# Performance work log

Hardware: AMD Instinct MI355X
Metric: run time of the kernel (lower is better)

The kernel has to match this reference:

```python
import jax, jax.numpy as jnp
import numpy as np

D_MODEL = 1024
D_HIDDEN = 4096
NUM_EXPERTS = 8
K_ACTIVE = 2


def setup_inputs() -> dict:
    key = jax.random.key(0)
    ks = jax.random.split(key, 8)
    x = jax.random.normal(ks[0], (1, 2048, D_MODEL), dtype=jnp.float32)
    gate_w = jax.random.normal(ks[1], (D_MODEL, NUM_EXPERTS), dtype=jnp.float32) * 0.02
    gate_b = jnp.zeros((NUM_EXPERTS,), dtype=jnp.float32)
    w1 = jax.random.normal(ks[2], (NUM_EXPERTS, D_MODEL, D_HIDDEN), dtype=jnp.float32) * 0.02
    b1 = jnp.zeros((NUM_EXPERTS, D_HIDDEN), dtype=jnp.float32)
    w2 = jax.random.normal(ks[3], (NUM_EXPERTS, D_HIDDEN, D_MODEL), dtype=jnp.float32) * 0.02
    b2 = jnp.zeros((NUM_EXPERTS, D_MODEL), dtype=jnp.float32)
    return {"x": x, "gate_w": gate_w, "gate_b": gate_b,
            "w1": w1, "b1": b1, "w2": w2, "b2": b2}


def reference(x, gate_w, gate_b, w1, b1, w2, b2):
    B, S, D = x.shape
    xf = x.reshape(-1, D)                                    # [T, D]
    logits = xf @ gate_w + gate_b                            # [T, E]
    top_w, top_idx = jax.lax.top_k(logits, K_ACTIVE)         # [T, K]
    top_w = jax.nn.softmax(top_w, axis=-1)                   # softmax over selected experts
    # combine-weight per expert: sum over k slots of one-hot(idx) * weight -> [T, E]
    gates = jnp.sum(jax.nn.one_hot(top_idx, NUM_EXPERTS, dtype=xf.dtype) * top_w[..., None], axis=1)
    # expert FFN applied per expert (dropout is identity in eval): gelu is exact (erf), matching torch nn.GELU default
    h = jax.nn.gelu(jnp.einsum('td,edh->teh', xf, w1) + b1[None], approximate=False)  # [T, E, H]
    y = jnp.einsum('teh,ehd->ted', h, w2) + b2[None]         # [T, E, D]
    out = jnp.einsum('ted,te->td', y, gates)                 # weighted combine of selected experts
    return out.reshape(B, S, D)
```

## Files before the change

### kernel.cpp

```cpp
#include <hip/hip_runtime.h>
#include <stdint.h>

typedef unsigned short u16;
typedef __attribute__((ext_vector_type(8))) short s16x8;
typedef __attribute__((ext_vector_type(8))) u16  u16x8;
typedef __attribute__((ext_vector_type(4))) float f32x4;

#define T_TOKENS 2048
#define DM 1024
#define DH 4096
#define NE 8
#define BM 128
#define BN 128
#define BK 64
#define MAXSLOTS (T_TOKENS*2 + NE*BM)
#define ROWBLK (MAXSLOTS/BM)

__device__ __forceinline__ u16 f2bf(float f) {
    union { float ff; uint32_t u; } v; v.ff = f;
    uint32_t r = v.u + 0x7fffu + ((v.u >> 16) & 1u);
    return (u16)(r >> 16);
}

#define GLOAD_LDS16(gsrc, ldst) \
    __builtin_amdgcn_global_load_lds((const __attribute__((address_space(1))) uint32_t*)(gsrc), \
                                     (__attribute__((address_space(3))) uint32_t*)(ldst), 16, 0, 0)

__global__ void k_convert(const float* __restrict__ x, u16* __restrict__ xbf,
                          int* __restrict__ ctrl) {
    int i = blockIdx.x * blockDim.x + threadIdx.x;
    const f32x4* xv = (const f32x4*)x;
    f32x4 a = xv[2*i], b = xv[2*i+1];
    u16x8 o;
    o[0]=f2bf(a[0]); o[1]=f2bf(a[1]); o[2]=f2bf(a[2]); o[3]=f2bf(a[3]);
    o[4]=f2bf(b[0]); o[5]=f2bf(b[1]); o[6]=f2bf(b[2]); o[7]=f2bf(b[3]);
    ((u16x8*)xbf)[i] = o;
    if (blockIdx.x == 0 && threadIdx.x < 32) ctrl[threadIdx.x] = 0;
}

__global__ void __launch_bounds__(64) k_gate(const float* __restrict__ x,
                                             const float* __restrict__ gw,
                                             const float* __restrict__ gb,
                                             int* __restrict__ cnt,
                                             int* __restrict__ tt_idx,
                                             float* __restrict__ tt_w) {
    const int t = blockIdx.x;
    const int lane = threadIdx.x;
    float acc[NE] = {0.f,0.f,0.f,0.f,0.f,0.f,0.f,0.f};
    const float* xr = x + (size_t)t * DM;
    #pragma unroll
    for (int c = 0; c < DM/64; ++c) {
        float xv = xr[lane + 64*c];
        const float* g = gw + (size_t)(lane + 64*c) * NE;
        #pragma unroll
        for (int e = 0; e < NE; ++e) acc[e] += xv * g[e];
    }
    #pragma unroll
    for (int e = 0; e < NE; ++e) {
        #pragma unroll
        for (int off = 32; off >= 1; off >>= 1)
            acc[e] += __shfl_xor(acc[e], off, 64);
    }
    if (lane == 0) {
        float l[NE];
        #pragma unroll
        for (int e = 0; e < NE; ++e) l[e] = acc[e] + gb[e];
        int i0 = 0;
        #pragma unroll
        for (int e = 1; e < NE; ++e) if (l[e] > l[i0]) i0 = e;
        int i1 = (i0 == 0) ? 1 : 0;
        #pragma unroll
        for (int e = 0; e < NE; ++e) if (e != i0 && l[e] > l[i1]) i1 = e;
        float m  = l[i0];
        float w0 = expf(l[i0] - m), w1 = expf(l[i1] - m);
        float s = w0 + w1; w0 /= s; w1 /= s;
        tt_idx[t*2] = i0; tt_idx[t*2+1] = i1;
        tt_w[t*2] = w0;  tt_w[t*2+1] = w1;
        atomicAdd(&cnt[i0], 1); atomicAdd(&cnt[i1], 1);
    }
}

__global__ void k_offsets(const int* __restrict__ cnt, int* __restrict__ fill,
                          int* __restrict__ off) {
    if (threadIdx.x == 0 && blockIdx.x == 0) {
        int a = 0;
        for (int e = 0; e < NE; ++e) {
            off[e] = a;
            a += (cnt[e] + BM - 1) / BM * BM;
            fill[e] = 0;
        }
        off[NE] = a;
    }
}

__global__ void k_scatter(const int* __restrict__ tt_idx, const float* __restrict__ tt_w,
                          const int* __restrict__ off, int* __restrict__ fill,
                          int* __restrict__ slot_token, float* __restrict__ slot_gate) {
    int t = blockIdx.x * blockDim.x + threadIdx.x;
    if (t >= T_TOKENS) return;
    #pragma unroll
    for (int k = 0; k < 2; ++k) {
        int e = tt_idx[t*2+k];
        int pos = off[e] + atomicAdd(&fill[e], 1);
        slot_token[pos] = t;
        slot_gate[pos]  = tt_w[t*2+k];
    }
}

__global__ void __launch_bounds__(256) k_ffn1(
    const u16* __restrict__ xbf, const float* __restrict__ w1,
    const float* __restrict__ b1, const int* __restrict__ slot_token,
    const int* __restrict__ off, u16* __restrict__ h)
{
    __shared__ u16 As[BM*BK];
    __shared__ u16 Bs[BN*BK];
    const int rb = blockIdx.y, cb = blockIdx.x;
    const int total = off[NE];
    const int r0 = rb * BM;
    if (r0 >= total) return;
    int e = 0;
    while (e < NE-1 && off[e+1] <= r0) e++;
    const float* Bsrc = w1 + (size_t)e * DM * DH;
    const float* be   = b1 + (size_t)e * DH;

    const int tid = threadIdx.x;
    const int lane = tid & 63, wid = tid >> 6;
    const int wr = wid >> 1, wc = wid & 1;

    const u16* gA[4];
    #pragma unroll
    for (int i = 0; i < 4; ++i) {
        int row = wid*32 + i*8 + (lane >> 3);
        int g = (lane & 7) ^ (row & 7);
        int tok = slot_token[r0 + row];
        gA[i] = xbf + (size_t)tok * DM + g*8;
    }
    const int tc = tid & 31, tr = tid >> 5;
    const float* gB = Bsrc + (size_t)(tr*8) * DH + cb*BN + tc*4;

    f32x4 acc[4][4];
    #pragma unroll
    for (int m = 0; m < 4; ++m)
        #pragma unroll
        for (int n = 0; n < 4; ++n) acc[m][n] = (f32x4){0.f,0.f,0.f,0.f};

    for (int kt = 0; kt < DM/BK; ++kt) {
        #pragma unroll
        for (int i = 0; i < 4; ++i)
            GLOAD_LDS16(gA[i] + kt*BK, &As[(wid*32 + i*8)*BK]);
        f32x4 bv[8];
        #pragma unroll
        for (int j = 0; j < 8; ++j)
            bv[j] = *(const f32x4*)(gB + (size_t)(kt*BK + j) * DH);
        #pragma unroll
        for (int c = 0; c < 4; ++c) {
            int n = tc*4 + c;
            int sl = tr ^ (n & 7);
            s16x8 pk;
            #pragma unroll
            for (int j = 0; j < 8; ++j) pk[j] = (short)f2bf(bv[j][c]);
            *(s16x8*)&Bs[n*BK + sl*8] = pk;
        }
        __syncthreads();
        #pragma unroll
        for (int ko = 0; ko < 2; ++ko) {
            s16x8 af[4], bfr[4];
            #pragma unroll
            for (int m = 0; m < 4; ++m) {
                int row = wr*64 + m*16 + (lane & 15);
                int sl = (ko*4 + (lane >> 4)) ^ (row & 7);
                af[m] = *(const s16x8*)&As[row*BK + sl*8];
            }
            #pragma unroll
            for (int n = 0; n < 4; ++n) {
                int col = wc*64 + n*16 + (lane & 15);
                int sl = (ko*4 + (lane >> 4)) ^ (col & 7);
                bfr[n] = *(const s16x8*)&Bs[col*BK + sl*8];
            }
            #pragma unroll
            for (int m = 0; m < 4; ++m)
                #pragma unroll
                for (int n = 0; n < 4; ++n)
                    acc[m][n] = __builtin_amdgcn_mfma_f32_16x16x32_bf16(af[m], bfr[n], acc[m][n], 0, 0, 0);
        }
        __syncthreads();
    }
    #pragma unroll
    for (int n = 0; n < 4; ++n) {
        int col = cb*BN + wc*64 + n*16 + (lane & 15);
        float bb = be[col];
        #pragma unroll
        for (int m = 0; m < 4; ++m) {
            int rbase = r0 + wr*64 + m*16 + (lane >> 4)*4;
            #pragma unroll
            for (int i = 0; i < 4; ++i) {
                float v = acc[m][n][i] + bb;
                float gv = 0.5f * v * (1.0f + erff(v * 0.70710678118654752f));
                h[(size_t)(rbase + i)*DH + col] = f2bf(gv);
            }
        }
    }
}

__global__ void __launch_bounds__(256) k_ffn2(
    const u16* __restrict__ h, const float* __restrict__ w2,
    const float* __restrict__ b2, const int* __restrict__ slot_token,
    const float* __restrict__ slot_gate, const int* __restrict__ off,
    float* __restrict__ out)
{
    __shared__ u16 As[BM*BK];
    __shared__ u16 Bs[BN*BK];
    const int rb = blockIdx.y, cb = blockIdx.x;
    const int total = off[NE];
    const int r0 = rb * BM;
    if (r0 >= total) return;
    int e = 0;
    while (e < NE-1 && off[e+1] <= r0) e++;
    const float* Bsrc = w2 + (size_t)e * DH * DM;
    const float* be   = b2 + (size_t)e * DM;

    const int tid = threadIdx.x;
    const int lane = tid & 63, wid = tid >> 6;
    const int wr = wid >> 1, wc = wid & 1;

    const u16* gA[4];
    #pragma unroll
    for (int i = 0; i < 4; ++i) {
        int row = wid*32 + i*8 + (lane >> 3);
        int g = (lane & 7) ^ (row & 7);
        gA[i] = h + (size_t)(r0 + row) * DH + g*8;
    }
    const int tc = tid & 31, tr = tid >> 5;
    const float* gB = Bsrc + (size_t)(tr*8) * DM + cb*BN + tc*4;

    f32x4 acc[4][4];
    #pragma unroll
    for (int m = 0; m < 4; ++m)
        #pragma unroll
        for (int n = 0; n < 4; ++n) acc[m][n] = (f32x4){0.f,0.f,0.f,0.f};

    for (int kt = 0; kt < DH/BK; ++kt) {
        #pragma unroll
        for (int i = 0; i < 4; ++i)
            GLOAD_LDS16(gA[i] + kt*BK, &As[(wid*32 + i*8)*BK]);
        f32x4 bv[8];
        #pragma unroll
        for (int j = 0; j < 8; ++j)
            bv[j] = *(const f32x4*)(gB + (size_t)(kt*BK + j) * DM);
        #pragma unroll
        for (int c = 0; c < 4; ++c) {
            int n = tc*4 + c;
            int sl = tr ^ (n & 7);
            s16x8 pk;
            #pragma unroll
            for (int j = 0; j < 8; ++j) pk[j] = (short)f2bf(bv[j][c]);
            *(s16x8*)&Bs[n*BK + sl*8] = pk;
        }
        __syncthreads();
        #pragma unroll
        for (int ko = 0; ko < 2; ++ko) {
            s16x8 af[4], bfr[4];
            #pragma unroll
            for (int m = 0; m < 4; ++m) {
                int row = wr*64 + m*16 + (lane & 15);
                int sl = (ko*4 + (lane >> 4)) ^ (row & 7);
                af[m] = *(const s16x8*)&As[row*BK + sl*8];
            }
            #pragma unroll
            for (int n = 0; n < 4; ++n) {
                int col = wc*64 + n*16 + (lane & 15);
                int sl = (ko*4 + (lane >> 4)) ^ (col & 7);
                bfr[n] = *(const s16x8*)&Bs[col*BK + sl*8];
            }
            #pragma unroll
            for (int m = 0; m < 4; ++m)
                #pragma unroll
                for (int n = 0; n < 4; ++n)
                    acc[m][n] = __builtin_amdgcn_mfma_f32_16x16x32_bf16(af[m], bfr[n], acc[m][n], 0, 0, 0);
        }
        __syncthreads();
    }
    float bb[4];
    #pragma unroll
    for (int n = 0; n < 4; ++n) bb[n] = be[cb*BN + wc*64 + n*16 + (lane & 15)];
    #pragma unroll
    for (int m = 0; m < 4; ++m) {
        #pragma unroll
        for (int i = 0; i < 4; ++i) {
            int s = r0 + wr*64 + m*16 + (lane >> 4)*4 + i;
            int tok = slot_token[s];
            float g = slot_gate[s];
            if (g != 0.0f) {
                float* orow = out + (size_t)tok * DM + cb*BN + wc*64;
                #pragma unroll
                for (int n = 0; n < 4; ++n)
                    atomicAdd(orow + n*16 + (lane & 15), g * (acc[m][n][i] + bb[n]));
            }
        }
    }
}

extern "C" void kernel_launch(void* const* d_in, const int* in_sizes, int n_in,
                              void* d_out, int out_size, void* d_ws, size_t ws_size,
                              hipStream_t stream)
{
    (void)in_sizes; (void)n_in; (void)out_size; (void)ws_size;
    const float* x  = (const float*)d_in[0];
    const float* gw = (const float*)d_in[1];
    const float* gb = (const float*)d_in[2];
    const float* w1 = (const float*)d_in[3];
    const float* b1 = (const float*)d_in[4];
    const float* w2 = (const float*)d_in[5];
    const float* b2 = (const float*)d_in[6];
    float* out = (float*)d_out;
    char* ws = (char*)d_ws;

    u16*   xbf        = (u16*)(ws);
    u16*   h          = (u16*)(ws + 4194304);
    int*   slot_token = (int*)(ws + 46137344);
    float* slot_gate  = (float*)(ws + 46157824);
    int*   tt_idx     = (int*)(ws + 46178304);
    float* tt_w       = (float*)(ws + 46194688);
    int*   ctrl       = (int*)(ws + 46211072);
    int* cnt = ctrl; int* fill = ctrl + 8; int* offs = ctrl + 16;

    hipMemsetAsync(slot_token, 0, 2 * MAXSLOTS * 4, stream);
    hipMemsetAsync(out, 0, (size_t)T_TOKENS * DM * sizeof(float), stream);

    k_convert<<<(T_TOKENS*DM/8 + 255)/256, 256, 0, stream>>>(x, xbf, ctrl);
    k_gate<<<T_TOKENS, 64, 0, stream>>>(x, gw, gb, cnt, tt_idx, tt_w);
    k_offsets<<<1, 64, 0, stream>>>(cnt, fill, offs);
    k_scatter<<<(T_TOKENS + 255)/256, 256, 0, stream>>>(tt_idx, tt_w, offs, fill, slot_token, slot_gate);
    k_ffn1<<<dim3(DH/BN, ROWBLK), 256, 0, stream>>>(xbf, w1, b1, slot_token, offs, h);
    k_ffn2<<<dim3(DM/BN, ROWBLK), 256, 0, stream>>>(h, w2, b2, slot_token, slot_gate, offs, out);
}
```

Before: 351.1 us.

## Pre-transpose expert weights to bf16 and stream them via LDS-direct loads

```diff
diff --git a/kernel.cpp b/kernel.cpp
--- a/kernel.cpp
+++ b/kernel.cpp
@@ -4,6 +4,7 @@
 typedef unsigned short u16;
 typedef __attribute__((ext_vector_type(8))) short s16x8;
 typedef __attribute__((ext_vector_type(8))) u16  u16x8;
+typedef __attribute__((ext_vector_type(4))) u16  u16x4;
 typedef __attribute__((ext_vector_type(4))) float f32x4;
 
 #define T_TOKENS 2048
@@ -12,6 +13,7 @@
 #define NE 8
 #define BM 128
 #define BN 128
+#define BN2 64
 #define BK 64
 #define MAXSLOTS (T_TOKENS*2 + NE*BM)
 #define ROWBLK (MAXSLOTS/BM)
@@ -38,6 +40,33 @@
     if (blockIdx.x == 0 && threadIdx.x < 32) ctrl[threadIdx.x] = 0;
 }
 
+__global__ void __launch_bounds__(256) k_transpose(const float* __restrict__ src,
+                                                   u16* __restrict__ dst,
+                                                   int K, int N) {
+    __shared__ float tile[64][65];
+    const int e = blockIdx.z;
+    const int n0 = blockIdx.x * 64, k0 = blockIdx.y * 64;
+    const float* s = src + (size_t)e * K * N;
+    u16* d = dst + (size_t)e * K * N;
+    const int tx = threadIdx.x & 15, ty = threadIdx.x >> 4;
+    #pragma unroll
+    for (int j = 0; j < 4; ++j) {
+        int r = ty * 4 + j;
+        f32x4 v = *(const f32x4*)(s + (size_t)(k0 + r) * N + n0 + tx * 4);
+        tile[r][tx*4+0] = v[0]; tile[r][tx*4+1] = v[1];
+        tile[r][tx*4+2] = v[2]; tile[r][tx*4+3] = v[3];
+    }
+    __syncthreads();
+    #pragma unroll
+    for (int j = 0; j < 4; ++j) {
+        int n = ty * 4 + j;
+        u16x4 w;
+        #pragma unroll
+        for (int c = 0; c < 4; ++c) w[c] = f2bf(tile[tx*4+c][n]);
+        *(u16x4*)(d + (size_t)(n0 + n) * K + k0 + tx * 4) = w;
+    }
+}
+
 __global__ void __launch_bounds__(64) k_gate(const float* __restrict__ x,
                                              const float* __restrict__ gw,
                                              const float* __restrict__ gb,
@@ -107,7 +136,184 @@
     }
 }
 
-__global__ void __launch_bounds__(256) k_ffn1(
+
+__global__ void __launch_bounds__(256) k_ffn1_b16(
+    const u16* __restrict__ xbf, const u16* __restrict__ w1t,
+    const float* __restrict__ b1, const int* __restrict__ slot_token,
+    const int* __restrict__ off, u16* __restrict__ h)
+{
+    __shared__ u16 As[BM*BK];
+    __shared__ u16 Bs[BN*BK];
+    const int rb = blockIdx.y, cb = blockIdx.x;
+    const int total = off[NE];
+    const int r0 = rb * BM;
+    if (r0 >= total) return;
+    int e = 0;
+    while (e < NE-1 && off[e+1] <= r0) e++;
+    const u16* Bsrc = w1t + (size_t)e * DM * DH;
+    const float* be = b1 + (size_t)e * DH;
+
+    const int tid = threadIdx.x;
+    const int lane = tid & 63, wid = tid >> 6;
+    const int wr = wid >> 1, wc = wid & 1;
+
+    const u16* gA[4]; const u16* gB[4];
+    #pragma unroll
+    for (int i = 0; i < 4; ++i) {
+        int row = wid*32 + i*8 + (lane >> 3);
+        int g = (lane & 7) ^ (row & 7);
+        int tok = slot_token[r0 + row];
+        gA[i] = xbf + (size_t)tok * DM + g*8;
+        gB[i] = Bsrc + (size_t)(cb*BN + row) * DM + g*8;
+    }
+
+    f32x4 acc[4][4];
+    #pragma unroll
+    for (int m = 0; m < 4; ++m)
+        #pragma unroll
+        for (int n = 0; n < 4; ++n) acc[m][n] = (f32x4){0.f,0.f,0.f,0.f};
+
+    for (int kt = 0; kt < DM/BK; ++kt) {
+        #pragma unroll
+        for (int i = 0; i < 4; ++i) {
+            GLOAD_LDS16(gA[i] + kt*BK, &As[(wid*32 + i*8)*BK]);
+            GLOAD_LDS16(gB[i] + kt*BK, &Bs[(wid*32 + i*8)*BK]);
+        }
+        __syncthreads();
+        #pragma unroll
+        for (int ko = 0; ko < 2; ++ko) {
+            s16x8 af[4], bfr[4];
+            #pragma unroll
+            for (int m = 0; m < 4; ++m) {
+                int row = wr*64 + m*16 + (lane & 15);
+                int sl = (ko*4 + (lane >> 4)) ^ (row & 7);
+                af[m] = *(const s16x8*)&As[row*BK + sl*8];
+            }
+            #pragma unroll
+            for (int n = 0; n < 4; ++n) {
+                int col = wc*64 + n*16 + (lane & 15);
+                int sl = (ko*4 + (lane >> 4)) ^ (col & 7);
+                bfr[n] = *(const s16x8*)&Bs[col*BK + sl*8];
+            }
+            #pragma unroll
+            for (int m = 0; m < 4; ++m)
+                #pragma unroll
+                for (int n = 0; n < 4; ++n)
+                    acc[m][n] = __builtin_amdgcn_mfma_f32_16x16x32_bf16(af[m], bfr[n], acc[m][n], 0, 0, 0);
+        }
+        __syncthreads();
+    }
+    #pragma unroll
+    for (int n = 0; n < 4; ++n) {
+        int col = cb*BN + wc*64 + n*16 + (lane & 15);
+        float bb = be[col];
+        #pragma unroll
+        for (int m = 0; m < 4; ++m) {
+            int rbase = r0 + wr*64 + m*16 + (lane >> 4)*4;
+            #pragma unroll
+            for (int i = 0; i < 4; ++i) {
+                float v = acc[m][n][i] + bb;
+                float gv = 0.5f * v * (1.0f + erff(v * 0.70710678118654752f));
+                h[(size_t)(rbase + i)*DH + col] = f2bf(gv);
+            }
+        }
+    }
+}
+
+__global__ void __launch_bounds__(256) k_ffn2_b16(
+    const u16* __restrict__ h, const u16* __restrict__ w2t,
+    const float* __restrict__ b2, const int* __restrict__ slot_token,
+    const float* __restrict__ slot_gate, const int* __restrict__ off,
+    float* __restrict__ out)
+{
+    __shared__ u16 As[BM*BK];
+    __shared__ u16 Bs[BN2*BK];
+    const int rb = blockIdx.y, cb = blockIdx.x;
+    const int total = off[NE];
+    const int r0 = rb * BM;
+    if (r0 >= total) return;
+    int e = 0;
+    while (e < NE-1 && off[e+1] <= r0) e++;
+    const u16* Bsrc = w2t + (size_t)e * DH * DM;
+    const float* be = b2 + (size_t)e * DM;
+
+    const int tid = threadIdx.x;
+    const int lane = tid & 63, wid = tid >> 6;
+    const int wr = wid >> 1, wc = wid & 1;
+
+    const u16* gA[4]; const u16* gB[2];
+    #pragma unroll
+    for (int i = 0; i < 4; ++i) {
+        int row = wid*32 + i*8 + (lane >> 3);
+        int g = (lane & 7) ^ (row & 7);
+        gA[i] = h + (size_t)(r0 + row) * DH + g*8;
+    }
+    #pragma unroll
+    for (int i = 0; i < 2; ++i) {
+        int n = wid*16 + i*8 + (lane >> 3);
+        int g = (lane & 7) ^ (n & 7);
+        gB[i] = Bsrc + (size_t)(cb*BN2 + n) * DH + g*8;
+    }
+
+    f32x4 acc[4][2];
+    #pragma unroll
+    for (int m = 0; m < 4; ++m)
+        #pragma unroll
+        for (int n = 0; n < 2; ++n) acc[m][n] = (f32x4){0.f,0.f,0.f,0.f};
+
+    for (int kt = 0; kt < DH/BK; ++kt) {
+        #pragma unroll
+        for (int i = 0; i < 4; ++i)
+            GLOAD_LDS16(gA[i] + kt*BK, &As[(wid*32 + i*8)*BK]);
+        #pragma unroll
+        for (int i = 0; i < 2; ++i)
+            GLOAD_LDS16(gB[i] + kt*BK, &Bs[(wid*16 + i*8)*BK]);
+        __syncthreads();
+        #pragma unroll
+        for (int ko = 0; ko < 2; ++ko) {
+            s16x8 af[4], bfr[2];
+            #pragma unroll
+            for (int m = 0; m < 4; ++m) {
+                int row = wr*64 + m*16 + (lane & 15);
+                int sl = (ko*4 + (lane >> 4)) ^ (row & 7);
+                af[m] = *(const s16x8*)&As[row*BK + sl*8];
+            }
+            #pragma unroll
+            for (int n = 0; n < 2; ++n) {
+                int col = wc*32 + n*16 + (lane & 15);
+                int sl = (ko*4 + (lane >> 4)) ^ (col & 7);
+                bfr[n] = *(const s16x8*)&Bs[col*BK + sl*8];
+            }
+            #pragma unroll
+            for (int m = 0; m < 4; ++m)
+                #pragma unroll
+                for (int n = 0; n < 2; ++n)
+                    acc[m][n] = __builtin_amdgcn_mfma_f32_16x16x32_bf16(af[m], bfr[n], acc[m][n], 0, 0, 0);
+        }
+        __syncthreads();
+    }
+    float bb[2];
+    #pragma unroll
+    for (int n = 0; n < 2; ++n) bb[n] = be[cb*BN2 + wc*32 + n*16 + (lane & 15)];
+    #pragma unroll
+    for (int m = 0; m < 4; ++m) {
+        #pragma unroll
+        for (int i = 0; i < 4; ++i) {
+            int s = r0 + wr*64 + m*16 + (lane >> 4)*4 + i;
+            int tok = slot_token[s];
+            float g = slot_gate[s];
+            if (g != 0.0f) {
+                float* orow = out + (size_t)tok * DM + cb*BN2 + wc*32;
+                #pragma unroll
+                for (int n = 0; n < 2; ++n)
+                    atomicAdd(orow + n*16 + (lane & 15), g * (acc[m][n][i] + bb[n]));
+            }
+        }
+    }
+}
+
+
+__global__ void __launch_bounds__(256) k_ffn1_f32(
     const u16* __restrict__ xbf, const float* __restrict__ w1,
     const float* __restrict__ b1, const int* __restrict__ slot_token,
     const int* __restrict__ off, u16* __restrict__ h)
@@ -202,7 +408,7 @@
     }
 }
 
-__global__ void __launch_bounds__(256) k_ffn2(
+__global__ void __launch_bounds__(256) k_ffn2_f32(
     const u16* __restrict__ h, const float* __restrict__ w2,
     const float* __restrict__ b2, const int* __restrict__ slot_token,
     const float* __restrict__ slot_gate, const int* __restrict__ off,
@@ -304,7 +510,7 @@
                               void* d_out, int out_size, void* d_ws, size_t ws_size,
                               hipStream_t stream)
 {
-    (void)in_sizes; (void)n_in; (void)out_size; (void)ws_size;
+    (void)in_sizes; (void)n_in; (void)out_size;
     const float* x  = (const float*)d_in[0];
     const float* gw = (const float*)d_in[1];
     const float* gb = (const float*)d_in[2];
@@ -315,22 +521,57 @@
     float* out = (float*)d_out;
     char* ws = (char*)d_ws;
 
-    u16*   xbf        = (u16*)(ws);
-    u16*   h          = (u16*)(ws + 4194304);
-    int*   slot_token = (int*)(ws + 46137344);
-    float* slot_gate  = (float*)(ws + 46157824);
-    int*   tt_idx     = (int*)(ws + 46178304);
-    float* tt_w       = (float*)(ws + 46194688);
-    int*   ctrl       = (int*)(ws + 46211072);
-    int* cnt = ctrl; int* fill = ctrl + 8; int* offs = ctrl + 16;
-
-    hipMemsetAsync(slot_token, 0, 2 * MAXSLOTS * 4, stream);
-    hipMemsetAsync(out, 0, (size_t)T_TOKENS * DM * sizeof(float), stream);
-
-    k_convert<<<(T_TOKENS*DM/8 + 255)/256, 256, 0, stream>>>(x, xbf, ctrl);
-    k_gate<<<T_TOKENS, 64, 0, stream>>>(x, gw, gb, cnt, tt_idx, tt_w);
-    k_offsets<<<1, 64, 0, stream>>>(cnt, fill, offs);
-    k_scatter<<<(T_TOKENS + 255)/256, 256, 0, stream>>>(tt_idx, tt_w, offs, fill, slot_token, slot_gate);
-    k_ffn1<<<dim3(DH/BN, ROWBLK), 256, 0, stream>>>(xbf, w1, b1, slot_token, offs, h);
-    k_ffn2<<<dim3(DM/BN, ROWBLK), 256, 0, stream>>>(h, w2, b2, slot_token, slot_gate, offs, out);
-}
+    const size_t OFF_XBF = 0;
+    const size_t OFF_H   = 4194304;
+    const size_t OFF_WT  = OFF_H + (size_t)MAXSLOTS * DH * 2;
+    const size_t OFF_ST  = OFF_WT + (size_t)NE * DM * DH * 2;
+    const size_t OFF_SG  = OFF_ST + MAXSLOTS * 4;
+    const size_t OFF_TI  = OFF_SG + MAXSLOTS * 4;
+    const size_t OFF_TW  = OFF_TI + T_TOKENS * 2 * 4;
+    const size_t OFF_CT  = OFF_TW + T_TOKENS * 2 * 4;
+    const size_t NEED_B16 = OFF_CT + 128;
+
+    if (ws_size >= NEED_B16) {
+        u16*   xbf        = (u16*)(ws + OFF_XBF);
+        u16*   h          = (u16*)(ws + OFF_H);
+        u16*   wt         = (u16*)(ws + OFF_WT);
+        int*   slot_token = (int*)(ws + OFF_ST);
+        float* slot_gate  = (float*)(ws + OFF_SG);
+        int*   tt_idx     = (int*)(ws + OFF_TI);
+        float* tt_w       = (float*)(ws + OFF_TW);
+        int*   ctrl       = (int*)(ws + OFF_CT);
+        int* cnt = ctrl; int* fill = ctrl + 8; int* offs = ctrl + 16;
+
+        hipMemsetAsync(slot_token, 0, 2 * MAXSLOTS * 4, stream);
+        hipMemsetAsync(out, 0, (size_t)T_TOKENS * DM * sizeof(float), stream);
+
+        k_convert<<<(T_TOKENS*DM/8 + 255)/256, 256, 0, stream>>>(x, xbf, ctrl);
+        k_gate<<<T_TOKENS, 64, 0, stream>>>(x, gw, gb, cnt, tt_idx, tt_w);
+        k_offsets<<<1, 64, 0, stream>>>(cnt, fill, offs);
+        k_scatter<<<(T_TOKENS + 255)/256, 256, 0, stream>>>(tt_idx, tt_w, offs, fill, slot_token, slot_gate);
+
+        k_transpose<<<dim3(DH/64, DM/64, NE), 256, 0, stream>>>(w1, wt, DM, DH);
+        k_ffn1_b16<<<dim3(DH/BN, ROWBLK), 256, 0, stream>>>(xbf, wt, b1, slot_token, offs, h);
+        k_transpose<<<dim3(DM/64, DH/64, NE), 256, 0, stream>>>(w2, wt, DH, DM);
+        k_ffn2_b16<<<dim3(DM/BN2, ROWBLK), 256, 0, stream>>>(h, wt, b2, slot_token, slot_gate, offs, out);
+    } else {
+        u16*   xbf        = (u16*)(ws);
+        u16*   h          = (u16*)(ws + 4194304);
+        int*   slot_token = (int*)(ws + 46137344);
+        float* slot_gate  = (float*)(ws + 46157824);
+        int*   tt_idx     = (int*)(ws + 46178304);
+        float* tt_w       = (float*)(ws + 46194688);
+        int*   ctrl       = (int*)(ws + 46211072);
+        int* cnt = ctrl; int* fill = ctrl + 8; int* offs = ctrl + 16;
+
+        hipMemsetAsync(slot_token, 0, 2 * MAXSLOTS * 4, stream);
+        hipMemsetAsync(out, 0, (size_t)T_TOKENS * DM * sizeof(float), stream);
+
+        k_convert<<<(T_TOKENS*DM/8 + 255)/256, 256, 0, stream>>>(x, xbf, ctrl);
+        k_gate<<<T_TOKENS, 64, 0, stream>>>(x, gw, gb, cnt, tt_idx, tt_w);
+        k_offsets<<<1, 64, 0, stream>>>(cnt, fill, offs);
+        k_scatter<<<(T_TOKENS + 255)/256, 256, 0, stream>>>(tt_idx, tt_w, offs, fill, slot_token, slot_gate);
+        k_ffn1_f32<<<dim3(DH/BN, ROWBLK), 256, 0, stream>>>(xbf, w1, b1, slot_token, offs, h);
+        k_ffn2_f32<<<dim3(DM/BN, ROWBLK), 256, 0, stream>>>(h, w2, b2, slot_token, slot_gate, offs, out);
+    }
+}
```

Result: faster. 311.8 us (-11.2%).
